# Kernel optimization log

Hardware: AMD Instinct MI355X
Metric: run time of the kernel (lower is better)

The kernel has to match this reference:

```python
import jax, jax.numpy as jnp
import numpy as np

B, T, D, H, L = 32, 2048, 512, 512, 2
G = 4 * H


def _lstm_layer(x, h0, c0, Wih, Whh, bih, bhh):
    """Run one LSTM layer over time, vectorized across batch.

    x: [B, T, D_in]; h0, c0: [H] (shared initial state across batch, as in the
    original module where every batch element reuses the same `states[i]`).
    Returns (ys [B, T, H], hT [B, H], cT [B, H]).
    """
    b = x.shape[0]
    # Precompute the input contribution to the gates for all timesteps at once
    # (the only part that doesn't depend on the recurrence): [B, T, 4H]
    xg = jnp.einsum('btd,gd->btg', x, Wih) + (bih + bhh)
    h_init = jnp.broadcast_to(h0, (b, H))
    c_init = jnp.broadcast_to(c0, (b, H))

    def step(carry, xg_t):
        h, c = carry  # [B, H] each
        gates = xg_t + h @ Whh.T  # [B, 4H]
        i, f, g, o = jnp.split(gates, 4, axis=-1)  # torch LSTMCell gate order
        c = jax.nn.sigmoid(f) * c + jax.nn.sigmoid(i) * jnp.tanh(g)
        h = jax.nn.sigmoid(o) * jnp.tanh(c)
        return (h, c), h

    (hT, cT), ys = jax.lax.scan(step, (h_init, c_init), jnp.swapaxes(xg, 0, 1))
    return jnp.swapaxes(ys, 0, 1), hT, cT  # ys -> [B, T, H]


def setup_inputs() -> dict:
    key = jax.random.key(0)
    ks = jax.random.split(key, 9)
    s_in = 1.0 / np.sqrt(H)
    inp = {
        'x': jax.random.normal(ks[0], (B, T, D), jnp.float32),
        'Wih0': jax.random.normal(ks[1], (G, D), jnp.float32) * s_in,
        'Whh0': jax.random.normal(ks[2], (G, H), jnp.float32) * s_in,
        'bih0': jax.random.normal(ks[3], (G,), jnp.float32) * s_in,
        'bhh0': jax.random.normal(ks[4], (G,), jnp.float32) * s_in,
        'Wih1': jax.random.normal(ks[5], (G, H), jnp.float32) * s_in,
        'Whh1': jax.random.normal(ks[6], (G, H), jnp.float32) * s_in,
        'bih1': jax.random.normal(ks[7], (G,), jnp.float32) * s_in,
        'bhh1': jax.random.normal(ks[8], (G,), jnp.float32) * s_in,
        'h0': jnp.zeros((L, H), jnp.float32),
        'c0': jnp.zeros((L, H), jnp.float32),
    }
    return inp


def reference(x, Wih0, Whh0, bih0, bhh0, Wih1, Whh1, bih1, bhh1, h0, c0):
    # Layer 0
    y, h_f0, c_f0 = _lstm_layer(x, h0[0], c0[0], Wih0, Whh0, bih0, bhh0)
    # Layer 1 (no dropout: dropout_probability=None)
    y, h_f1, c_f1 = _lstm_layer(y, h0[1], c0[1], Wih1, Whh1, bih1, bhh1)
    h_final = jnp.stack([h_f0, h_f1])  # [L, B, H]
    c_final = jnp.stack([c_f0, c_f1])  # [L, B, H]
    return y, h_final, c_final
```

## Files before the change

### kernel.cpp

```cpp
#include <hip/hip_runtime.h>

namespace {
constexpr int TT  = 2048;
constexpr int NBL = 64;
constexpr size_t YSZ = (size_t)32 * TT * 512;
constexpr size_t HFO = YSZ;
constexpr size_t CFO = YSZ + (size_t)2 * 32 * 512;
constexpr int O_WLO  = 65536;
constexpr int O_GA   = 131072;
constexpr int O_XGB  = 139776;
constexpr int O_HOUT = 157184;
constexpr int O_LF   = 157696;
constexpr int TILE_F = 272;
constexpr int LF_GA = 0, LF_XF = 4, LF_XC = 8;
}

typedef float f32x4 __attribute__((ext_vector_type(4)));
typedef short s16x8 __attribute__((ext_vector_type(8)));

__device__ __forceinline__ float sigf(float v)  { return 1.0f / (1.0f + __expf(-v)); }
__device__ __forceinline__ float tanh_(float v) { return 1.0f - 2.0f / (__expf(2.0f * v) + 1.0f); }
__device__ __forceinline__ short f2bf(float v) {
  unsigned u = __float_as_uint(v);
  u += 0x7FFFu + ((u >> 16) & 1u);
  return (short)(u >> 16);
}
__device__ __forceinline__ float bf2f(short h) {
  return __uint_as_float(((unsigned)(unsigned short)h) << 16);
}
__device__ __forceinline__ s16x8 cvt8hi(const f32x4& p, const f32x4& q) {
  s16x8 r;
  r[0] = f2bf(p.x); r[1] = f2bf(p.y); r[2] = f2bf(p.z); r[3] = f2bf(p.w);
  r[4] = f2bf(q.x); r[5] = f2bf(q.y); r[6] = f2bf(q.z); r[7] = f2bf(q.w);
  return r;
}
__device__ __forceinline__ s16x8 ld_bf8_coh(const void* p) {
  s16x8 r;
  asm volatile("global_load_dwordx4 %0, %1, off sc1" : "=v"(r) : "v"(p) : "memory");
  return r;
}
__device__ __forceinline__ void st_b16_coh(void* p, s16x8 v) {
  asm volatile("global_store_dwordx4 %0, %1, off sc1" :: "v"(p), "v"(v) : "memory");
}
__device__ __forceinline__ void st_flag(int* p, int v) {
  __hip_atomic_store(p, v, __ATOMIC_RELAXED, __HIP_MEMORY_SCOPE_AGENT);
}
__device__ __forceinline__ void poll_ge(const int* f, int need) {
  while (__hip_atomic_load(f, __ATOMIC_RELAXED, __HIP_MEMORY_SCOPE_AGENT) < need)
    __builtin_amdgcn_s_sleep(1);
}
__device__ __forceinline__ void lspin_ge(int* p, int need) {
  while (__hip_atomic_load(p, __ATOMIC_ACQUIRE, __HIP_MEMORY_SCOPE_WORKGROUP) < need)
    __builtin_amdgcn_s_sleep(0);
  __builtin_amdgcn_sched_barrier(0);
}
__device__ __forceinline__ void lset(int* p, int v) {
  __hip_atomic_store(p, v, __ATOMIC_RELEASE, __HIP_MEMORY_SCOPE_WORKGROUP);
}

#define VMCNT0() do { asm volatile("s_waitcnt vmcnt(0)" ::: "memory"); __builtin_amdgcn_sched_barrier(0); } while (0)
#define LGKM0()  do { asm volatile("s_waitcnt lgkmcnt(0)" ::: "memory"); __builtin_amdgcn_sched_barrier(0); } while (0)

#define MFMA __builtin_amdgcn_mfma_f32_16x16x32_bf16

__global__ __launch_bounds__(512)
void lstm_persist(
    const float* __restrict__ x,
    const float* __restrict__ Wih0, const float* __restrict__ Whh0,
    const float* __restrict__ bih0, const float* __restrict__ bhh0,
    const float* __restrict__ Wih1, const float* __restrict__ Whh1,
    const float* __restrict__ bih1, const float* __restrict__ bhh1,
    const float* __restrict__ h0c, const float* __restrict__ c0c,
    float* __restrict__ out,
    short* __restrict__ r0hi, short* __restrict__ r1hi,
    int* __restrict__ flags0, int* __restrict__ flags1)
{
  __shared__ __align__(16) char LDS[157760];
  char* Whi = LDS;
  char* Wlo = LDS + O_WLO;
  float* gAp = (float*)(LDS + O_GA);
  float* xgp = (float*)(LDS + O_XGB);
  int* lf = (int*)(LDS + O_LF);

  const int tid   = (int)threadIdx.x;
  const int lane  = tid & 63;
  const int w     = tid >> 6;
  const int layer = (int)(blockIdx.x >> 6);
  const int lb    = (int)(blockIdx.x & (NBL - 1));
  const int j0    = lb << 3;
  const bool isA  = (w < 4);

  const float* Wih = layer ? Wih1 : Wih0;
  const float* Whh = layer ? Whh1 : Whh0;
  const float* bih = layer ? bih1 : bih0;
  const float* bhh = layer ? bhh1 : bhh0;
  short* rhiO = layer ? r1hi : r0hi;
  int* flO = layer ? flags1 : flags0;
  const int rmask = layer ? 3 : 7;

  for (int idx = tid; idx < 32 * 1024; idx += 512) {
    const int row = idx >> 10;
    const int k   = idx & 1023;
    const int rg  = ((row >> 3) << 9) + j0 + (row & 7);
    const float vv = (k < 512) ? Wih[(rg << 9) + k] : Whh[(rg << 9) + (k - 512)];
    const short h = f2bf(vv);
    const short l = f2bf(vv - bf2f(h));
    const int byte = (row << 11) + ((k << 1) ^ ((row & 15) << 4));
    *(short*)(Whi + byte) = h;
    *(short*)(Wlo + byte) = l;
  }
  for (int i = tid; i < 2048; i += 512) {
    const int b = i >> 6, c8 = i & 63;
    const float* hp = h0c + layer * 512 + (c8 << 3);
    const f32x4 p = *(const f32x4*)hp;
    const f32x4 q = *(const f32x4*)(hp + 4);
    st_b16_coh((char*)rhiO + (rmask << 15) + (b << 10) + (c8 << 4), cvt8hi(p, q));
  }
  VMCNT0();
  if (tid == 0) {
    st_flag(flO + lb, 1);
#pragma unroll
    for (int i = 0; i < 16; ++i) lf[i] = 0;
  }
  float creg = 0.0f;
  float bias_[4] = {0.f, 0.f, 0.f, 0.f};
  int jjC = 0, bC = 0;
  if (isA) {
    jjC = tid >> 5;
    bC  = tid & 31;
    creg = c0c[layer * 512 + j0 + jjC];
#pragma unroll
    for (int g = 0; g < 4; ++g) bias_[g] = bih[(g << 9) + j0 + jjC] + bhh[(g << 9) + j0 + jjC];
  }
  LGKM0();
  __builtin_amdgcn_s_barrier();
  __builtin_amdgcn_sched_barrier(0);

  const int kg = lane >> 4;

  if (isA) {
    const int bg = w & 1, kh = w >> 1;
    const int b_ld = (bg << 4) + (lane & 15);
    const int colb = (kh << 8) + (kg << 3);
#pragma unroll 1
    for (int s = 0; s < TT; ++s) {
      poll_ge(flO + lane, s + 1);
      const int rslot = (s + rmask) & rmask;
      s16x8 bh[8];
      const char* pb = (const char*)rhiO + (rslot << 15) + (b_ld << 10) + (colb << 1);
#pragma unroll
      for (int ks = 0; ks < 8; ++ks) bh[ks] = ld_bf8_coh(pb + (ks << 6));
      VMCNT0();
      f32x4 acc[2][2];
#pragma unroll
      for (int rg = 0; rg < 2; ++rg)
#pragma unroll
        for (int p = 0; p < 2; ++p) acc[rg][p] = (f32x4){0.f, 0.f, 0.f, 0.f};
#pragma unroll
      for (int ks = 0; ks < 8; ++ks)
#pragma unroll
        for (int rg = 0; rg < 2; ++rg) {
          const int wrow = (rg << 4) + (lane & 15);
          const int wk = 512 + (kh << 8) + (ks << 5) + (kg << 3);
          const int wb = (wrow << 11) + ((wk << 1) ^ ((wrow & 15) << 4));
          acc[rg][ks & 1] = MFMA(*(const s16x8*)(Whi + wb), bh[ks], acc[rg][ks & 1], 0, 0, 0);
          acc[rg][ks & 1] = MFMA(*(const s16x8*)(Wlo + wb), bh[ks], acc[rg][ks & 1], 0, 0, 0);
        }
#pragma unroll
      for (int rg = 0; rg < 2; ++rg) {
        const f32x4 c = acc[rg][0] + acc[rg][1];
        float* tp = gAp + ((kh << 2) + (rg << 1) + bg) * TILE_F + (kg << 2) * 17 + (lane & 15);
#pragma unroll
        for (int r = 0; r < 4; ++r) tp[r * 17] = c[r];
      }
      LGKM0();
      lset(&lf[LF_GA + w], s + 1);
#pragma unroll
      for (int i = 0; i < 4; ++i) lspin_ge(&lf[LF_GA + i], s + 1);
#pragma unroll
      for (int i = 0; i < 4; ++i) lspin_ge(&lf[LF_XF + i], s + 1);
      const float* xgs = xgp + (s & 1) * 2176;
      float gv[4];
#pragma unroll
      for (int g = 0; g < 4; ++g) {
        const int row = (g << 3) + jjC;
        const int base = (((row >> 4) << 1) + (bC >> 4)) * TILE_F + (row & 15) * 17 + (bC & 15);
        gv[g] = gAp[base] + gAp[base + 4 * TILE_F] + xgs[base] + xgs[base + 4 * TILE_F] + bias_[g];
      }
      const float cn = sigf(gv[1]) * creg + sigf(gv[0]) * tanh_(gv[2]);
      const float hn = sigf(gv[3]) * tanh_(cn);
      creg = cn;
      if (layer == 1) out[((size_t)((bC << 11) + s) << 9) + j0 + jjC] = hn;
      if (s == TT - 1) out[HFO + (size_t)(((layer << 5) + bC) << 9) + j0 + jjC] = hn;
      *(short*)(LDS + O_HOUT + (bC << 4) + (jjC << 1)) = f2bf(hn);
      LGKM0();
      lset(&lf[LF_XC + w], s + 1);
      if (w == 0) {
        lspin_ge(&lf[LF_XC + 1], s + 1);
        lspin_ge(&lf[LF_XC + 2], s + 1);
        lspin_ge(&lf[LF_XC + 3], s + 1);
        if (layer == 0 && s >= 8) poll_ge(flags1 + lane, s - 6);
        if (lane < 32) {
          const s16x8 hv = *(const s16x8*)(LDS + O_HOUT + (lane << 4));
          st_b16_coh((char*)rhiO + ((s & rmask) << 15) + (lane << 10) + (j0 << 1), hv);
        }
        VMCNT0();
        if (lane == 0) st_flag(flO + lb, s + 2);
      }
    }
    out[CFO + (size_t)(((layer << 5) + bC) << 9) + j0 + jjC] = creg;
  } else {
    const int v = w - 4;
    const int bg = v & 1, kh = v >> 1;
    const int b_ld = (bg << 4) + (lane & 15);
    const int colb = (kh << 8) + (kg << 3);
#pragma unroll 1
    for (int t = 0; t < TT; ++t) {
#pragma unroll
      for (int i = 0; i < 4; ++i) lspin_ge(&lf[LF_XC + i], t - 1);
      f32x4 acc[2][2];
#pragma unroll
      for (int rg = 0; rg < 2; ++rg)
#pragma unroll
        for (int p = 0; p < 2; ++p) acc[rg][p] = (f32x4){0.f, 0.f, 0.f, 0.f};
      if (layer == 0) {
#pragma unroll 1
        for (int round = 0; round < 2; ++round) {
          f32x4 xr[8];
#pragma unroll
          for (int i = 0; i < 8; ++i) {
            const int ks = (round << 2) + (i >> 1);
            const int col = colb + (ks << 5) + ((i & 1) << 2);
            xr[i] = *(const f32x4*)(x + ((size_t)((b_ld << 11) + t) << 9) + col);
          }
#pragma unroll
          for (int sl = 0; sl < 4; ++sl) {
            const int ks = (round << 2) + sl;
            const s16x8 bh = cvt8hi(xr[sl << 1], xr[(sl << 1) + 1]);
#pragma unroll
            for (int rg = 0; rg < 2; ++rg) {
              const int wrow = (rg << 4) + (lane & 15);
              const int wk = (kh << 8) + (ks << 5) + (kg << 3);
              const int wb = (wrow << 11) + ((wk << 1) ^ ((wrow & 15) << 4));
              acc[rg][ks & 1] = MFMA(*(const s16x8*)(Whi + wb), bh, acc[rg][ks & 1], 0, 0, 0);
              acc[rg][ks & 1] = MFMA(*(const s16x8*)(Wlo + wb), bh, acc[rg][ks & 1], 0, 0, 0);
            }
          }
        }
      } else {
        poll_ge(flags0 + lane, t + 2);
        s16x8 bh[8];
        const char* pb = (const char*)r0hi + ((t & 7) << 15) + (b_ld << 10) + (colb << 1);
#pragma unroll
        for (int ks = 0; ks < 8; ++ks) bh[ks] = ld_bf8_coh(pb + (ks << 6));
        VMCNT0();
#pragma unroll
        for (int ks = 0; ks < 8; ++ks)
#pragma unroll
          for (int rg = 0; rg < 2; ++rg) {
            const int wrow = (rg << 4) + (lane & 15);
            const int wk = (kh << 8) + (ks << 5) + (kg << 3);
            const int wb = (wrow << 11) + ((wk << 1) ^ ((wrow & 15) << 4));
            acc[rg][ks & 1] = MFMA(*(const s16x8*)(Whi + wb), bh[ks], acc[rg][ks & 1], 0, 0, 0);
            acc[rg][ks & 1] = MFMA(*(const s16x8*)(Wlo + wb), bh[ks], acc[rg][ks & 1], 0, 0, 0);
          }
      }
      float* xps = xgp + (t & 1) * 2176;
#pragma unroll
      for (int rg = 0; rg < 2; ++rg) {
        const f32x4 c = acc[rg][0] + acc[rg][1];
        float* tp = xps + ((kh << 2) + (rg << 1) + bg) * TILE_F + (kg << 2) * 17 + (lane & 15);
#pragma unroll
        for (int r = 0; r < 4; ++r) tp[r * 17] = c[r];
      }
      LGKM0();
      lset(&lf[LF_XF + v], t + 1);
    }
  }
}

extern "C" void kernel_launch(void* const* d_in, const int* in_sizes, int n_in,
                              void* d_out, int out_size, void* d_ws, size_t ws_size,
                              hipStream_t stream) {
  (void)in_sizes; (void)n_in; (void)out_size; (void)ws_size;
  const float* x    = (const float*)d_in[0];
  const float* Wih0 = (const float*)d_in[1];
  const float* Whh0 = (const float*)d_in[2];
  const float* bih0 = (const float*)d_in[3];
  const float* bhh0 = (const float*)d_in[4];
  const float* Wih1 = (const float*)d_in[5];
  const float* Whh1 = (const float*)d_in[6];
  const float* bih1 = (const float*)d_in[7];
  const float* bhh1 = (const float*)d_in[8];
  const float* h0   = (const float*)d_in[9];
  const float* c0   = (const float*)d_in[10];

  float* out = (float*)d_out;
  short* r0hi = (short*)d_ws;
  short* r1hi = (short*)((char*)d_ws + (256 << 10));
  int* flags0 = (int*)((char*)d_ws + (384 << 10));
  int* flags1 = (int*)((char*)d_ws + (384 << 10) + 256);

  hipMemsetAsync(flags0, 0, 512, stream);

  hipLaunchKernelGGL(lstm_persist, dim3(2 * NBL), dim3(512), 0, stream,
                     x, Wih0, Whh0, bih0, bhh0, Wih1, Whh1, bih1, bhh1,
                     h0, c0, out, r0hi, r1hi, flags0, flags1);
}
```

Baseline: 19.22 ms.

## Embed step tags in hidden-state packets to replace separate flag polling

```diff
diff --git a/kernel.cpp b/kernel.cpp
--- a/kernel.cpp
+++ b/kernel.cpp
@@ -17,6 +17,7 @@
 
 typedef float f32x4 __attribute__((ext_vector_type(4)));
 typedef short s16x8 __attribute__((ext_vector_type(8)));
+typedef int   i32x4 __attribute__((ext_vector_type(4)));
 
 __device__ __forceinline__ float sigf(float v)  { return 1.0f / (1.0f + __expf(-v)); }
 __device__ __forceinline__ float tanh_(float v) { return 1.0f - 2.0f / (__expf(2.0f * v) + 1.0f); }
@@ -34,13 +35,18 @@
   r[4] = f2bf(q.x); r[5] = f2bf(q.y); r[6] = f2bf(q.z); r[7] = f2bf(q.w);
   return r;
 }
-__device__ __forceinline__ s16x8 ld_bf8_coh(const void* p) {
-  s16x8 r;
+__device__ __forceinline__ i32x4 ld_pkt(const void* p) {
+  i32x4 r;
   asm volatile("global_load_dwordx4 %0, %1, off sc1" : "=v"(r) : "v"(p) : "memory");
   return r;
 }
-__device__ __forceinline__ void st_b16_coh(void* p, s16x8 v) {
+__device__ __forceinline__ void st_pkt(void* p, i32x4 v) {
   asm volatile("global_store_dwordx4 %0, %1, off sc1" :: "v"(p), "v"(v) : "memory");
+}
+__device__ __forceinline__ s16x8 mk_bh(i32x4 a, i32x4 b) {
+  i32x4 t;
+  t[0] = a[0]; t[1] = a[1]; t[2] = b[0]; t[3] = b[1];
+  return __builtin_bit_cast(s16x8, t);
 }
 __device__ __forceinline__ void st_flag(int* p, int v) {
   __hip_atomic_store(p, v, __ATOMIC_RELAXED, __HIP_MEMORY_SCOPE_AGENT);
@@ -72,8 +78,7 @@
     const float* __restrict__ bih1, const float* __restrict__ bhh1,
     const float* __restrict__ h0c, const float* __restrict__ c0c,
     float* __restrict__ out,
-    short* __restrict__ r0hi, short* __restrict__ r1hi,
-    int* __restrict__ flags0, int* __restrict__ flags1)
+    char* __restrict__ ring0, char* __restrict__ ring1, int* __restrict__ flags1)
 {
   __shared__ __align__(16) char LDS[157760];
   char* Whi = LDS;
@@ -94,8 +99,7 @@
   const float* Whh = layer ? Whh1 : Whh0;
   const float* bih = layer ? bih1 : bih0;
   const float* bhh = layer ? bhh1 : bhh0;
-  short* rhiO = layer ? r1hi : r0hi;
-  int* flO = layer ? flags1 : flags0;
+  char* rO = layer ? ring1 : ring0;
   const int rmask = layer ? 3 : 7;
 
   for (int idx = tid; idx < 32 * 1024; idx += 512) {
@@ -109,16 +113,16 @@
     *(short*)(Whi + byte) = h;
     *(short*)(Wlo + byte) = l;
   }
-  for (int i = tid; i < 2048; i += 512) {
-    const int b = i >> 6, c8 = i & 63;
-    const float* hp = h0c + layer * 512 + (c8 << 3);
-    const f32x4 p = *(const f32x4*)hp;
-    const f32x4 q = *(const f32x4*)(hp + 4);
-    st_b16_coh((char*)rhiO + (rmask << 15) + (b << 10) + (c8 << 4), cvt8hi(p, q));
-  }
-  VMCNT0();
+  if (w == 0) {
+    const int b = lane >> 1, g = lane & 1;
+    const float* hp = h0c + layer * 512 + j0 + (g << 2);
+    i32x4 pkt;
+    pkt[0] = (int)(unsigned short)f2bf(hp[0]) | ((int)(unsigned short)f2bf(hp[1]) << 16);
+    pkt[1] = (int)(unsigned short)f2bf(hp[2]) | ((int)(unsigned short)f2bf(hp[3]) << 16);
+    pkt[2] = 1; pkt[3] = 0;
+    st_pkt(rO + (rmask << 16) + (b << 11) + (lb << 5) + (g << 4), pkt);
+  }
   if (tid == 0) {
-    st_flag(flO + lb, 1);
 #pragma unroll
     for (int i = 0; i < 16; ++i) lf[i] = 0;
   }
@@ -141,31 +145,40 @@
   if (isA) {
     const int bg = w & 1, kh = w >> 1;
     const int b_ld = (bg << 4) + (lane & 15);
-    const int colb = (kh << 8) + (kg << 3);
 #pragma unroll 1
     for (int s = 0; s < TT; ++s) {
-      poll_ge(flO + lane, s + 1);
-      const int rslot = (s + rmask) & rmask;
-      s16x8 bh[8];
-      const char* pb = (const char*)rhiO + (rslot << 15) + (b_ld << 10) + (colb << 1);
-#pragma unroll
-      for (int ks = 0; ks < 8; ++ks) bh[ks] = ld_bf8_coh(pb + (ks << 6));
-      VMCNT0();
+      const char* hb = rO + ((((s - 1) & rmask)) << 16) + (b_ld << 11) + (kh << 10) + (kg << 5);
+      const int want = s + 1;
+      i32x4 gr[16];
+      while (true) {
+#pragma unroll
+        for (int ks = 0; ks < 8; ++ks) {
+          gr[2 * ks]     = ld_pkt(hb + (ks << 7));
+          gr[2 * ks + 1] = ld_pkt(hb + (ks << 7) + 16);
+        }
+        VMCNT0();
+        int bad = 0;
+#pragma unroll
+        for (int i = 0; i < 16; ++i) bad |= (gr[i][2] != want) ? 1 : 0;
+        if (!__any(bad)) break;
+      }
       f32x4 acc[2][2];
 #pragma unroll
       for (int rg = 0; rg < 2; ++rg)
 #pragma unroll
         for (int p = 0; p < 2; ++p) acc[rg][p] = (f32x4){0.f, 0.f, 0.f, 0.f};
 #pragma unroll
-      for (int ks = 0; ks < 8; ++ks)
+      for (int ks = 0; ks < 8; ++ks) {
+        const s16x8 bh = mk_bh(gr[2 * ks], gr[2 * ks + 1]);
 #pragma unroll
         for (int rg = 0; rg < 2; ++rg) {
           const int wrow = (rg << 4) + (lane & 15);
           const int wk = 512 + (kh << 8) + (ks << 5) + (kg << 3);
           const int wb = (wrow << 11) + ((wk << 1) ^ ((wrow & 15) << 4));
-          acc[rg][ks & 1] = MFMA(*(const s16x8*)(Whi + wb), bh[ks], acc[rg][ks & 1], 0, 0, 0);
-          acc[rg][ks & 1] = MFMA(*(const s16x8*)(Wlo + wb), bh[ks], acc[rg][ks & 1], 0, 0, 0);
-        }
+          acc[rg][ks & 1] = MFMA(*(const s16x8*)(Whi + wb), bh, acc[rg][ks & 1], 0, 0, 0);
+          acc[rg][ks & 1] = MFMA(*(const s16x8*)(Wlo + wb), bh, acc[rg][ks & 1], 0, 0, 0);
+        }
+      }
 #pragma unroll
       for (int rg = 0; rg < 2; ++rg) {
         const f32x4 c = acc[rg][0] + acc[rg][1];
@@ -199,13 +212,14 @@
         lspin_ge(&lf[LF_XC + 1], s + 1);
         lspin_ge(&lf[LF_XC + 2], s + 1);
         lspin_ge(&lf[LF_XC + 3], s + 1);
-        if (layer == 0 && s >= 8) poll_ge(flags1 + lane, s - 6);
-        if (lane < 32) {
-          const s16x8 hv = *(const s16x8*)(LDS + O_HOUT + (lane << 4));
-          st_b16_coh((char*)rhiO + ((s & rmask) << 15) + (lane << 10) + (j0 << 1), hv);
-        }
-        VMCNT0();
-        if (lane == 0) st_flag(flO + lb, s + 2);
+        if (layer == 0 && s >= 8) poll_ge(flags1 + lane, s - 7);
+        const int b = lane >> 1, g = lane & 1;
+        i32x4 pkt;
+        pkt[0] = *(const int*)(LDS + O_HOUT + (b << 4) + (g << 3));
+        pkt[1] = *(const int*)(LDS + O_HOUT + (b << 4) + (g << 3) + 4);
+        pkt[2] = s + 2; pkt[3] = 0;
+        st_pkt(rO + ((s & rmask) << 16) + (b << 11) + (lb << 5) + (g << 4), pkt);
+        if (layer == 1 && lane == 0) st_flag(flags1 + lb, s + 1);
       }
     }
     out[CFO + (size_t)(((layer << 5) + bC) << 9) + j0 + jjC] = creg;
@@ -213,7 +227,6 @@
     const int v = w - 4;
     const int bg = v & 1, kh = v >> 1;
     const int b_ld = (bg << 4) + (lane & 15);
-    const int colb = (kh << 8) + (kg << 3);
 #pragma unroll 1
     for (int t = 0; t < TT; ++t) {
 #pragma unroll
@@ -224,6 +237,7 @@
 #pragma unroll
         for (int p = 0; p < 2; ++p) acc[rg][p] = (f32x4){0.f, 0.f, 0.f, 0.f};
       if (layer == 0) {
+        const int colb = (kh << 8) + (kg << 3);
 #pragma unroll 1
         for (int round = 0; round < 2; ++round) {
           f32x4 xr[8];
@@ -248,22 +262,33 @@
           }
         }
       } else {
-        poll_ge(flags0 + lane, t + 2);
-        s16x8 bh[8];
-        const char* pb = (const char*)r0hi + ((t & 7) << 15) + (b_ld << 10) + (colb << 1);
-#pragma unroll
-        for (int ks = 0; ks < 8; ++ks) bh[ks] = ld_bf8_coh(pb + (ks << 6));
-        VMCNT0();
-#pragma unroll
-        for (int ks = 0; ks < 8; ++ks)
+        const char* yb = ring0 + (((t & 7)) << 16) + (b_ld << 11) + (kh << 10) + (kg << 5);
+        const int want = t + 2;
+        i32x4 gr[16];
+        while (true) {
+#pragma unroll
+          for (int ks = 0; ks < 8; ++ks) {
+            gr[2 * ks]     = ld_pkt(yb + (ks << 7));
+            gr[2 * ks + 1] = ld_pkt(yb + (ks << 7) + 16);
+          }
+          VMCNT0();
+          int bad = 0;
+#pragma unroll
+          for (int i = 0; i < 16; ++i) bad |= (gr[i][2] != want) ? 1 : 0;
+          if (!__any(bad)) break;
+        }
+#pragma unroll
+        for (int ks = 0; ks < 8; ++ks) {
+          const s16x8 bh = mk_bh(gr[2 * ks], gr[2 * ks + 1]);
 #pragma unroll
           for (int rg = 0; rg < 2; ++rg) {
             const int wrow = (rg << 4) + (lane & 15);
             const int wk = (kh << 8) + (ks << 5) + (kg << 3);
             const int wb = (wrow << 11) + ((wk << 1) ^ ((wrow & 15) << 4));
-            acc[rg][ks & 1] = MFMA(*(const s16x8*)(Whi + wb), bh[ks], acc[rg][ks & 1], 0, 0, 0);
-            acc[rg][ks & 1] = MFMA(*(const s16x8*)(Wlo + wb), bh[ks], acc[rg][ks & 1], 0, 0, 0);
+            acc[rg][ks & 1] = MFMA(*(const s16x8*)(Whi + wb), bh, acc[rg][ks & 1], 0, 0, 0);
+            acc[rg][ks & 1] = MFMA(*(const s16x8*)(Wlo + wb), bh, acc[rg][ks & 1], 0, 0, 0);
           }
+        }
       }
       float* xps = xgp + (t & 1) * 2176;
 #pragma unroll
@@ -296,14 +321,13 @@
   const float* c0   = (const float*)d_in[10];
 
   float* out = (float*)d_out;
-  short* r0hi = (short*)d_ws;
-  short* r1hi = (short*)((char*)d_ws + (256 << 10));
-  int* flags0 = (int*)((char*)d_ws + (384 << 10));
-  int* flags1 = (int*)((char*)d_ws + (384 << 10) + 256);
-
-  hipMemsetAsync(flags0, 0, 512, stream);
+  char* ring0 = (char*)d_ws;
+  char* ring1 = (char*)d_ws + (512 << 10);
+  int*  flags1 = (int*)((char*)d_ws + (768 << 10));
+
+  hipMemsetAsync(d_ws, 0, (768 << 10) + 4096, stream);
 
   hipLaunchKernelGGL(lstm_persist, dim3(2 * NBL), dim3(512), 0, stream,
                      x, Wih0, Whh0, bih0, bhh0, Wih1, Whh1, bih1, bhh1,
-                     h0, c0, out, r0hi, r1hi, flags0, flags1);
-}
+                     h0, c0, out, ring0, ring1, flags1);
+}
```

New measurement: 19.80 ms. 1.03x slower.
